# Kernel tuning notes

Hardware: AMD Instinct MI355X
Metric: run time of the kernel (lower is better)

## Reference

```python
import jax, jax.numpy as jnp
import numpy as np
jax.config.update("jax_enable_x64", True)

IN_FEATURES = 4096
OUT_FEATURES = 4096
BATCH, SEQ = 4, 2048


def _gen_weight(seed, out_features, in_features):
    # Stand-in for the Rust FastGMemContext PRNG fill: deterministic fp64
    # weight regenerated from the 64-bit seed on every call (never stored).
    k = jax.random.key(seed)
    return jax.random.normal(k, (out_features, in_features), dtype=jnp.float64)


def setup_inputs() -> dict:
    key = jax.random.key(0)
    kx, _ = jax.random.split(key)
    x = jax.random.normal(kx, (BATCH, SEQ, IN_FEATURES), dtype=jnp.float32)
    bias = jnp.zeros((OUT_FEATURES,), dtype=jnp.float32)
    return {"x": x, "bias": bias, "seed": 42}


def reference(x, bias, seed):
    out_features = bias.shape[0]
    in_features = x.shape[-1]
    w = _gen_weight(seed, out_features, in_features)  # [out, in] fp64
    # fp64 matmul, downcast to input dtype, then add bias (as in GMemLinear)
    out = jnp.matmul(x.astype(jnp.float64), w.T).astype(x.dtype)
    return out + bias
```

## Files before the change

### kernel.cpp

```cpp
#include <hip/hip_runtime.h>
#include <hip/hip_bf16.h>
#include <cstdint>
#include <math.h>


typedef __bf16  bf16x8 __attribute__((ext_vector_type(8)));
typedef float   f32x4  __attribute__((ext_vector_type(4)));
typedef unsigned short u16x8 __attribute__((ext_vector_type(8)));

__device__ __forceinline__ unsigned short f2bf_rne(float f) {
  uint32_t x = __float_as_uint(f);
  uint32_t r = (x + 0x7FFFu + ((x >> 16) & 1u)) >> 16;
  return (unsigned short)r;
}

__device__ __forceinline__ void threefry2x32(uint32_t k0, uint32_t k1,
                                             uint32_t x0, uint32_t x1,
                                             uint32_t& o0, uint32_t& o1) {
  uint32_t ks0 = k0, ks1 = k1, ks2 = k0 ^ k1 ^ 0x1BD11BDAu;
  uint32_t ks[3] = {ks0, ks1, ks2};
  x0 += ks0; x1 += ks1;
  const uint32_t rot0[4] = {13u, 15u, 26u, 6u};
  const uint32_t rot1[4] = {17u, 29u, 16u, 24u};
#pragma unroll
  for (int i = 0; i < 5; ++i) {
    const uint32_t* r = (i & 1) ? rot1 : rot0;
#pragma unroll
    for (int j = 0; j < 4; ++j) {
      x0 += x1;
      x1 = (x1 << r[j]) | (x1 >> (32u - r[j]));
      x1 ^= x0;
    }
    x0 += ks[(i + 1) % 3];
    x1 += ks[(i + 2) % 3] + (uint32_t)(i + 1);
  }
  o0 = x0; o1 = x1;
}

__device__ __forceinline__ double erfinv_mixed(double u) {
  double au = fabs(u);
  double t  = (1.0 - au) * (1.0 + au);
  float  wf = -logf((float)t);
  if (wf < 15.5f) {
    float w, p;
    if (wf < 5.0f) {
      w = wf - 2.5f;
      p = 2.81022636e-08f;
      p = 3.43273939e-07f + p * w;
      p = -3.5233877e-06f + p * w;
      p = -4.39150654e-06f + p * w;
      p = 0.00021858087f + p * w;
      p = -0.00125372503f + p * w;
      p = -0.00417768164f + p * w;
      p = 0.246640727f + p * w;
      p = 1.50140941f + p * w;
    } else {
      w = sqrtf(wf) - 3.0f;
      p = -0.000200214257f;
      p = 0.000100950558f + p * w;
      p = 0.00134934322f + p * w;
      p = -0.00367342844f + p * w;
      p = 0.00573950773f + p * w;
      p = -0.0076224613f + p * w;
      p = 0.00943887047f + p * w;
      p = 1.00167406f + p * w;
      p = 2.83297682f + p * w;
    }
    return (double)(p * (float)u);
  } else {
    double L = -log(1.0 - au);
    double r = sqrt(L);
    r = sqrt(L - log(r) - 0.5723649429247001);
    r = sqrt(L - log(r) - 0.5723649429247001);
    return (u < 0.0) ? -r : r;
  }
}

__global__ void genw_kernel(unsigned short* __restrict__ W,
                            const int* __restrict__ seedp, int total) {
  const uint32_t k1 = (uint32_t)seedp[0];
  const uint32_t k0 = 0u;
  const double DLO = -0x1.fffffffffffffp-1;
  const int nq = total >> 2;
  const int stride = (int)(gridDim.x * blockDim.x);
  for (int q = (int)(blockIdx.x * blockDim.x + threadIdx.x); q < nq; q += stride) {
    ushort4 outv;
    unsigned short tmp[4];
#pragma unroll
    for (int j = 0; j < 4; ++j) {
      uint32_t e = ((uint32_t)q << 2) + (uint32_t)j;
      uint32_t o0, o1;
      threefry2x32(k0, k1, 0u, e, o0, o1);
      uint64_t bits = ((uint64_t)o0 << 32) | (uint64_t)o1;
      uint64_t fb = (bits >> 12) | 0x3FF0000000000000ull;
      union { uint64_t u; double d; } cv; cv.u = fb;
      double f = cv.d - 1.0;
      double u = f * 2.0 + DLO;
      u = fmax(u, DLO);
      double x = erfinv_mixed(u);
      float wv = (float)(1.4142135623730951 * x);
      tmp[j] = f2bf_rne(wv);
    }
    outv.x = tmp[0]; outv.y = tmp[1]; outv.z = tmp[2]; outv.w = tmp[3];
    *(ushort4*)(W + ((size_t)q << 2)) = outv;
  }
}

__global__ void castx_kernel(const float* __restrict__ X,
                             unsigned short* __restrict__ Y, int n) {
  const int n8 = n >> 3;
  const int stride = (int)(gridDim.x * blockDim.x);
  for (int q = (int)(blockIdx.x * blockDim.x + threadIdx.x); q < n8; q += stride) {
    const float4* p = (const float4*)(X + ((size_t)q << 3));
    float4 a = p[0], b = p[1];
    u16x8 o;
    o[0] = f2bf_rne(a.x); o[1] = f2bf_rne(a.y);
    o[2] = f2bf_rne(a.z); o[3] = f2bf_rne(a.w);
    o[4] = f2bf_rne(b.x); o[5] = f2bf_rne(b.y);
    o[6] = f2bf_rne(b.z); o[7] = f2bf_rne(b.w);
    *(u16x8*)(Y + ((size_t)q << 3)) = o;
  }
}


__device__ __forceinline__ void gload_lds16(const void* g, void* l) {
  __builtin_amdgcn_global_load_lds(
      (const __attribute__((address_space(1))) unsigned int*)g,
      (__attribute__((address_space(3))) unsigned int*)l, 16, 0, 0);
}

__device__ __forceinline__ uint32_t lds_u32(void* p) {
  return (uint32_t)(uintptr_t)(__attribute__((address_space(3))) char*)p;
}

template <int OFF>
__device__ __forceinline__ bf16x8 dsr16(uint32_t a) {
  bf16x8 r;
  asm volatile("ds_read_b128 %0, %1 offset:%2" : "=v"(r) : "v"(a), "i"(OFF));
  return r;
}

__global__ __launch_bounds__(512, 2) void gemm256(
    const unsigned short* __restrict__ A,
    const unsigned short* __restrict__ B,
    const float* __restrict__ bias,
    float* __restrict__ C,
    int M, int N, int K) {
  __shared__ __align__(1024) char lds[131072];

  const int nwg = (int)gridDim.x;
  int wg = (int)blockIdx.x;
  wg = (wg & 7) * (nwg >> 3) + (wg >> 3);
  const int ntn = N >> 8;
  const int tm = wg / ntn, tn = wg - tm * ntn;

  const int tid = (int)threadIdx.x;
  const int w = tid >> 6, l = tid & 63;
  const int wr = w >> 2, wc = w & 3;
  const int l15 = l & 15;

  int laneRd = (l15 << 6) | ((l >> 4) << 4);
  laneRd ^= ((l15 >> 1) & 3) << 4;
  const int stRow = l >> 2;
  const int stCol = (((l & 3) ^ ((l >> 3) & 3)) << 4);

  const char* Ag = (const char*)A;
  const char* Bg = (const char*)B;
  const long rowA0 = (long)tm * 256;
  const long rowB0 = (long)tn * 256;
  const long Kb = (long)K;

  const uint32_t lds0  = lds_u32(&lds[0]);
  const uint32_t aBase = lds0 + (uint32_t)(wr * 16384 + laneRd);
  const uint32_t bBase = lds0 + 65536u + (uint32_t)(wc * 8192 + laneRd);

#define STAGE(kt_, c_)                                                        \
  {                                                                           \
    const long kb_ = (long)(kt_) * 64;                                        \
    char* Ab_ = &lds[(c_) * 32768];                                           \
    char* Bb_ = &lds[65536 + (c_) * 32768];                                   \
    _Pragma("unroll")                                                         \
    for (int i_ = 0; i_ < 4; ++i_) {                                          \
      const int u_ = w * 4 + i_;                                              \
      const int r4_ = u_ >> 1, s_ = u_ & 1;                                   \
      gload_lds16(Ag + 2 * ((rowA0 + r4_ * 16 + stRow) * Kb + kb_ + s_ * 32) + stCol, \
                  Ab_ + u_ * 1024);                                           \
      gload_lds16(Bg + 2 * ((rowB0 + r4_ * 16 + stRow) * Kb + kb_ + s_ * 32) + stCol, \
                  Bb_ + u_ * 1024);                                           \
    }                                                                         \
  }

#define BRD(base_)                                                            \
  bq[0][0] = dsr16<0>(base_);    bq[0][1] = dsr16<1024>(base_);               \
  bq[1][0] = dsr16<2048>(base_); bq[1][1] = dsr16<3072>(base_);               \
  bq[2][0] = dsr16<4096>(base_); bq[2][1] = dsr16<5120>(base_);               \
  bq[3][0] = dsr16<6144>(base_); bq[3][1] = dsr16<7168>(base_);

#define ARD(mi0_, base_)                                                      \
  aq[0][0] = dsr16<(mi0_) * 2048>(base_);                                     \
  aq[0][1] = dsr16<(mi0_) * 2048 + 1024>(base_);                              \
  aq[1][0] = dsr16<((mi0_) + 1) * 2048>(base_);                               \
  aq[1][1] = dsr16<((mi0_) + 1) * 2048 + 1024>(base_);

#define MFMA16(mi0_)                                                          \
  _Pragma("unroll")                                                           \
  for (int s = 0; s < 2; ++s)                                                 \
    _Pragma("unroll")                                                         \
    for (int dm = 0; dm < 2; ++dm)                                            \
      _Pragma("unroll")                                                       \
      for (int ni = 0; ni < 4; ++ni)                                          \
        acc[(mi0_) + dm][ni] = __builtin_amdgcn_mfma_f32_16x16x32_bf16(       \
            aq[dm][s], bq[ni][s], acc[(mi0_) + dm][ni], 0, 0, 0);

#define LGKM0_FENCE                                                           \
  asm volatile("s_waitcnt lgkmcnt(0)" ::: "memory");                          \
  __builtin_amdgcn_sched_barrier(0);

#define TILE_BODY(t_, c_)                                                     \
  {                                                                           \
    const uint32_t aB = aBase + (c_) * 32768u;                                \
    const uint32_t bB = bBase + (c_) * 32768u;                                \
    if ((t_) + 1 < NTt) { asm volatile("s_waitcnt vmcnt(8)" ::: "memory"); }  \
    else                { asm volatile("s_waitcnt vmcnt(0)" ::: "memory"); }  \
    __builtin_amdgcn_sched_barrier(0);                                        \
    __builtin_amdgcn_s_barrier();                                             \
    bf16x8 aq[2][2], bq[4][2];                                                \
    BRD(bB)                                                                   \
    ARD(0, aB)                                                                \
    __builtin_amdgcn_s_barrier();                                             \
    LGKM0_FENCE                                                               \
    __builtin_amdgcn_s_setprio(1);                                            \
    MFMA16(0)                                                                 \
    __builtin_amdgcn_s_setprio(0);                                            \
    __builtin_amdgcn_s_barrier();                                             \
    ARD(2, aB)                                                                \
    __builtin_amdgcn_s_barrier();                                             \
    LGKM0_FENCE                                                               \
    __builtin_amdgcn_s_setprio(1);                                            \
    MFMA16(2)                                                                 \
    __builtin_amdgcn_s_setprio(0);                                            \
    __builtin_amdgcn_s_barrier();                                             \
    ARD(4, aB)                                                                \
    __builtin_amdgcn_s_barrier();                                             \
    LGKM0_FENCE                                                               \
    __builtin_amdgcn_s_setprio(1);                                            \
    MFMA16(4)                                                                 \
    __builtin_amdgcn_s_setprio(0);                                            \
    __builtin_amdgcn_s_barrier();                                             \
    ARD(6, aB)                                                                \
    LGKM0_FENCE                                                               \
    __builtin_amdgcn_s_barrier();                                             \
    if ((t_) + 2 < NTt) STAGE((t_) + 2, c_)                                   \
    __builtin_amdgcn_sched_barrier(0);                                        \
    __builtin_amdgcn_s_setprio(1);                                            \
    MFMA16(6)                                                                 \
    __builtin_amdgcn_s_setprio(0);                                            \
  }

  f32x4 acc[8][4];
#pragma unroll
  for (int i = 0; i < 8; ++i)
#pragma unroll
    for (int j = 0; j < 4; ++j) acc[i][j] = (f32x4){0.f, 0.f, 0.f, 0.f};

  const int NTt = K >> 6;
  STAGE(0, 0)
  STAGE(1, 1)

  for (int t = 0; t < NTt; t += 2) {
    TILE_BODY(t, 0)
    TILE_BODY(t + 1, 1)
  }

#pragma unroll
  for (int ni = 0; ni < 4; ++ni) {
    const int col = tn * 256 + wc * 64 + ni * 16 + l15;
    const float bv = bias[col];
#pragma unroll
    for (int mi = 0; mi < 8; ++mi) {
      const int r0 = tm * 256 + wr * 128 + mi * 16 + ((l >> 4) << 2);
      f32x4 v = acc[mi][ni];
#pragma unroll
      for (int j = 0; j < 4; ++j)
        C[(size_t)(r0 + j) * N + col] = v[j] + bv;
    }
  }
#undef STAGE
#undef BRD
#undef ARD
#undef MFMA16
#undef LGKM0_FENCE
#undef TILE_BODY
}

extern "C" void kernel_launch(void* const* d_in, const int* in_sizes, int n_in,
                              void* d_out, int out_size, void* d_ws, size_t ws_size,
                              hipStream_t stream) {
  const float* x    = (const float*)d_in[0];
  const float* bias = (const float*)d_in[1];
  const int*   seed = (const int*)d_in[2];
  float* out = (float*)d_out;

  const int K = 4096;
  const int N = in_sizes[1];
  const int M = in_sizes[0] / K;

  unsigned short* W  = (unsigned short*)d_ws;
  unsigned short* Xb = W + (size_t)N * K;

  genw_kernel<<<8192, 256, 0, stream>>>(W, seed, N * K);
  castx_kernel<<<2048, 256, 0, stream>>>(x, Xb, M * K);

  dim3 grid((M / 256) * (N / 256));
  gemm256<<<grid, 512, 0, stream>>>((const unsigned short*)Xb,
                                    (const unsigned short*)W,
                                    bias, out, M, N, K);
}
```

Measured before the change: 355.5 us.

## Switch GEMM main loop to 4-stage K=32 pipeline with split A/B staging

```diff
diff --git a/kernel.cpp b/kernel.cpp
--- a/kernel.cpp
+++ b/kernel.cpp
@@ -171,90 +171,61 @@
   const long Kb = (long)K;
 
   const uint32_t lds0  = lds_u32(&lds[0]);
-  const uint32_t aBase = lds0 + (uint32_t)(wr * 16384 + laneRd);
-  const uint32_t bBase = lds0 + 65536u + (uint32_t)(wc * 8192 + laneRd);
-
-#define STAGE(kt_, c_)                                                        \
-  {                                                                           \
-    const long kb_ = (long)(kt_) * 64;                                        \
-    char* Ab_ = &lds[(c_) * 32768];                                           \
-    char* Bb_ = &lds[65536 + (c_) * 32768];                                   \
+  const uint32_t aBase = lds0 + (uint32_t)(wr * 8192 + laneRd);
+  const uint32_t bBase = lds0 + 16384u + (uint32_t)(wc * 4096 + laneRd);
+
+#define STAGE_A(kt_, cs_)                                                     \
+  _Pragma("unroll")                                                           \
+  for (int i_ = 0; i_ < 2; ++i_) {                                            \
+    const int u_ = w * 2 + i_;                                                \
+    gload_lds16(Ag + 2 * ((rowA0 + u_ * 16 + stRow) * Kb + (long)(kt_) * 32) + stCol, \
+                &lds[(cs_) * 32768 + u_ * 1024]);                             \
+  }
+#define STAGE_B(kt_, cs_)                                                     \
+  _Pragma("unroll")                                                           \
+  for (int i_ = 0; i_ < 2; ++i_) {                                            \
+    const int u_ = w * 2 + i_;                                                \
+    gload_lds16(Bg + 2 * ((rowB0 + u_ * 16 + stRow) * Kb + (long)(kt_) * 32) + stCol, \
+                &lds[(cs_) * 32768 + 16384 + u_ * 1024]);                     \
+  }
+
+#define MFMA16(base_)                                                         \
+  _Pragma("unroll")                                                           \
+  for (int mi = 0; mi < 4; ++mi)                                              \
     _Pragma("unroll")                                                         \
-    for (int i_ = 0; i_ < 4; ++i_) {                                          \
-      const int u_ = w * 4 + i_;                                              \
-      const int r4_ = u_ >> 1, s_ = u_ & 1;                                   \
-      gload_lds16(Ag + 2 * ((rowA0 + r4_ * 16 + stRow) * Kb + kb_ + s_ * 32) + stCol, \
-                  Ab_ + u_ * 1024);                                           \
-      gload_lds16(Bg + 2 * ((rowB0 + r4_ * 16 + stRow) * Kb + kb_ + s_ * 32) + stCol, \
-                  Bb_ + u_ * 1024);                                           \
-    }                                                                         \
-  }
-
-#define BRD(base_)                                                            \
-  bq[0][0] = dsr16<0>(base_);    bq[0][1] = dsr16<1024>(base_);               \
-  bq[1][0] = dsr16<2048>(base_); bq[1][1] = dsr16<3072>(base_);               \
-  bq[2][0] = dsr16<4096>(base_); bq[2][1] = dsr16<5120>(base_);               \
-  bq[3][0] = dsr16<6144>(base_); bq[3][1] = dsr16<7168>(base_);
-
-#define ARD(mi0_, base_)                                                      \
-  aq[0][0] = dsr16<(mi0_) * 2048>(base_);                                     \
-  aq[0][1] = dsr16<(mi0_) * 2048 + 1024>(base_);                              \
-  aq[1][0] = dsr16<((mi0_) + 1) * 2048>(base_);                               \
-  aq[1][1] = dsr16<((mi0_) + 1) * 2048 + 1024>(base_);
-
-#define MFMA16(mi0_)                                                          \
-  _Pragma("unroll")                                                           \
-  for (int s = 0; s < 2; ++s)                                                 \
-    _Pragma("unroll")                                                         \
-    for (int dm = 0; dm < 2; ++dm)                                            \
-      _Pragma("unroll")                                                       \
-      for (int ni = 0; ni < 4; ++ni)                                          \
-        acc[(mi0_) + dm][ni] = __builtin_amdgcn_mfma_f32_16x16x32_bf16(       \
-            aq[dm][s], bq[ni][s], acc[(mi0_) + dm][ni], 0, 0, 0);
-
-#define LGKM0_FENCE                                                           \
-  asm volatile("s_waitcnt lgkmcnt(0)" ::: "memory");                          \
-  __builtin_amdgcn_sched_barrier(0);
-
-#define TILE_BODY(t_, c_)                                                     \
+    for (int ni = 0; ni < 4; ++ni)                                            \
+      acc[(base_) + mi][ni] = __builtin_amdgcn_mfma_f32_16x16x32_bf16(        \
+          aq[mi], bq[ni], acc[(base_) + mi][ni], 0, 0, 0);
+
+#define TILE_BODY(c_, kt_, vm_, st_)                                          \
   {                                                                           \
     const uint32_t aB = aBase + (c_) * 32768u;                                \
     const uint32_t bB = bBase + (c_) * 32768u;                                \
-    if ((t_) + 1 < NTt) { asm volatile("s_waitcnt vmcnt(8)" ::: "memory"); }  \
-    else                { asm volatile("s_waitcnt vmcnt(0)" ::: "memory"); }  \
+    bf16x8 aq[4], bq[4];                                                      \
+    bq[0] = dsr16<0>(bB);    bq[1] = dsr16<1024>(bB);                         \
+    bq[2] = dsr16<2048>(bB); bq[3] = dsr16<3072>(bB);                         \
+    aq[0] = dsr16<0>(aB);    aq[1] = dsr16<1024>(aB);                         \
+    aq[2] = dsr16<2048>(aB); aq[3] = dsr16<3072>(aB);                         \
+    if (st_) { STAGE_A((kt_) + 3, ((c_) + 3) & 3) }                           \
+    __builtin_amdgcn_s_barrier();                                             \
+    asm volatile("s_waitcnt lgkmcnt(0)" ::: "memory");                        \
     __builtin_amdgcn_sched_barrier(0);                                        \
-    __builtin_amdgcn_s_barrier();                                             \
-    bf16x8 aq[2][2], bq[4][2];                                                \
-    BRD(bB)                                                                   \
-    ARD(0, aB)                                                                \
-    __builtin_amdgcn_s_barrier();                                             \
-    LGKM0_FENCE                                                               \
     __builtin_amdgcn_s_setprio(1);                                            \
     MFMA16(0)                                                                 \
     __builtin_amdgcn_s_setprio(0);                                            \
     __builtin_amdgcn_s_barrier();                                             \
-    ARD(2, aB)                                                                \
-    __builtin_amdgcn_s_barrier();                                             \
-    LGKM0_FENCE                                                               \
-    __builtin_amdgcn_s_setprio(1);                                            \
-    MFMA16(2)                                                                 \
-    __builtin_amdgcn_s_setprio(0);                                            \
-    __builtin_amdgcn_s_barrier();                                             \
-    ARD(4, aB)                                                                \
-    __builtin_amdgcn_s_barrier();                                             \
-    LGKM0_FENCE                                                               \
+    aq[0] = dsr16<4096>(aB); aq[1] = dsr16<5120>(aB);                         \
+    aq[2] = dsr16<6144>(aB); aq[3] = dsr16<7168>(aB);                         \
+    if (st_) { STAGE_B((kt_) + 3, ((c_) + 3) & 3) }                           \
+    __builtin_amdgcn_s_barrier();                                             \
+    asm volatile("s_waitcnt lgkmcnt(0)" ::: "memory");                        \
+    __builtin_amdgcn_sched_barrier(0);                                        \
     __builtin_amdgcn_s_setprio(1);                                            \
     MFMA16(4)                                                                 \
     __builtin_amdgcn_s_setprio(0);                                            \
-    __builtin_amdgcn_s_barrier();                                             \
-    ARD(6, aB)                                                                \
-    LGKM0_FENCE                                                               \
-    __builtin_amdgcn_s_barrier();                                             \
-    if ((t_) + 2 < NTt) STAGE((t_) + 2, c_)                                   \
+    asm volatile("s_waitcnt vmcnt(" #vm_ ")" ::: "memory");                   \
     __builtin_amdgcn_sched_barrier(0);                                        \
-    __builtin_amdgcn_s_setprio(1);                                            \
-    MFMA16(6)                                                                 \
-    __builtin_amdgcn_s_setprio(0);                                            \
+    __builtin_amdgcn_s_barrier();                                             \
   }
 
   f32x4 acc[8][4];
@@ -263,14 +234,26 @@
 #pragma unroll
     for (int j = 0; j < 4; ++j) acc[i][j] = (f32x4){0.f, 0.f, 0.f, 0.f};
 
-  const int NTt = K >> 6;
-  STAGE(0, 0)
-  STAGE(1, 1)
-
-  for (int t = 0; t < NTt; t += 2) {
-    TILE_BODY(t, 0)
-    TILE_BODY(t + 1, 1)
-  }
+  const int NTt = K >> 5;
+
+  STAGE_A(0, 0) STAGE_B(0, 0)
+  STAGE_A(1, 1) STAGE_B(1, 1)
+  STAGE_A(2, 2) STAGE_B(2, 2)
+  asm volatile("s_waitcnt vmcnt(8)" ::: "memory");
+  __builtin_amdgcn_sched_barrier(0);
+  __builtin_amdgcn_s_barrier();
+
+  int kt = 0;
+  for (; kt + 7 < NTt; kt += 4) {
+    TILE_BODY(0, kt,     8, 1)
+    TILE_BODY(1, kt + 1, 8, 1)
+    TILE_BODY(2, kt + 2, 8, 1)
+    TILE_BODY(3, kt + 3, 8, 1)
+  }
+  TILE_BODY(0, kt,     8, 1)
+  TILE_BODY(1, kt + 1, 4, 0)
+  TILE_BODY(2, kt + 2, 0, 0)
+  TILE_BODY(3, kt + 3, 0, 0)
 
 #pragma unroll
   for (int ni = 0; ni < 4; ++ni) {
@@ -285,11 +268,9 @@
         C[(size_t)(r0 + j) * N + col] = v[j] + bv;
     }
   }
-#undef STAGE
-#undef BRD
-#undef ARD
+#undef STAGE_A
+#undef STAGE_B
 #undef MFMA16
-#undef LGKM0_FENCE
 #undef TILE_BODY
 }
 
```

New measurement: 330.1 us. 1.08x faster.
